# Kernel optimization log

Hardware: AMD Instinct MI355X
Metric: run time of the kernel (lower is better)

Reference implementation:

```python
import jax, jax.numpy as jnp
import numpy as np

B, S, DIM = 2, 1024, 1024
N_EXPERTS, K = 8, 2
VOCAB = 16384
HIDDEN = DIM * 8 // 3          # 2730
UP_OUT = HIDDEN * 2            # 5460 (swiglu doubling)


def setup_inputs() -> dict:
    key = jax.random.key(0)
    ks = jax.random.split(key, 5)
    x = jax.random.normal(ks[0], (B, S, DIM), dtype=jnp.float32)
    w_router = jax.random.normal(ks[1], (N_EXPERTS, DIM), dtype=jnp.float32) * 0.02
    w_up = jax.random.normal(ks[2], (N_EXPERTS, UP_OUT, DIM), dtype=jnp.float32) * 0.02
    w_down = jax.random.normal(ks[3], (N_EXPERTS, DIM, HIDDEN), dtype=jnp.float32) * 0.02
    w_proj = jax.random.normal(ks[4], (N_EXPERTS, VOCAB, DIM), dtype=jnp.float32) * 0.02
    return {"x": x, "w_router": w_router, "w_up": w_up, "w_down": w_down, "w_proj": w_proj}


def _grouped_linear(x_sorted, weight, group_sizes):
    # weight: [n_experts, out, in] (torch Linear layout) -> ragged_dot wants [g, in, out]
    return jax.lax.ragged_dot(x_sorted, jnp.swapaxes(weight, 1, 2), group_sizes)


def reference(x, w_router, w_up, w_down, w_proj):
    b, s, d = x.shape
    # Router (eval path): plain top-k of linear scores
    scores = jnp.einsum("bsd,nd->bsn", x, w_router)
    c, ids = jax.lax.top_k(scores, K)                   # [B,S,K]
    # Dispatch: replicate tokens k times, sort by expert id (stable, matching torch.sort)
    xe = jnp.broadcast_to(x[..., None, :], (b, s, K, d)).reshape(-1, d)   # [T, d]
    ids_flat = ids.reshape(-1)
    order = jnp.argsort(ids_flat)                        # stable sort indices
    x_sorted = xe[order]
    group_sizes = jnp.bincount(ids_flat, length=N_EXPERTS).astype(jnp.int32)
    # Expert swiglu MLP with residual (grouped GEMMs)
    skip = x_sorted
    h = _grouped_linear(x_sorted, w_up, group_sizes)     # [T, 2*HIDDEN]
    h_lin, h_gate = jnp.split(h, 2, axis=-1)
    h = h_lin * jax.nn.silu(h_gate)
    h = _grouped_linear(h, w_down, group_sizes) + skip   # [T, d]
    logits = _grouped_linear(h, w_proj, group_sizes)     # [T, VOCAB]
    # Postprocess: scatter back to original token order
    out = jnp.zeros_like(logits).at[order].set(logits)
    out = out.reshape(b, s, K, VOCAB)
    # Weighted top-k combine
    w = jax.nn.softmax(c, axis=-1)                       # [B,S,K]
    return jnp.sum(out * w[..., None], axis=-2)          # [B,S,VOCAB]
```

## Files before the change

kernel.cpp:

```cpp
#include <hip/hip_runtime.h>
#include <hip/hip_bf16.h>

typedef __bf16 bf16_t;
typedef __bf16 bf16x2 __attribute__((ext_vector_type(2)));
typedef __bf16 bf16x4 __attribute__((ext_vector_type(4)));
typedef __bf16 bf16x8 __attribute__((ext_vector_type(8)));
typedef float f32x4 __attribute__((ext_vector_type(4)));

#define DIM     1024
#define NEXP    8
#define VOCAB   16384
#define HIDDEN  2730
#define UPOUT   5460
#define NTOK    2048
#define NSLOT   4096
#define HRAW_LD 5472
#define H1_LD   2752
#define BM      256
#define MAXTILES 24

#define WS_COUNTS      0
#define WS_NTILES      64
#define WS_TILE_E      128
#define WS_TILE_M0     384
#define WS_TILE_MEND   640
#define WS_SLOT_IDS    1024
#define WS_SLOT_W      17408
#define WS_SLOT_OF_POS 33792
#define WS_POS_OF_SLOT 50176
#define WS_XSORTED     66560
#define WS_H2          8455168
#define WS_H1          16843776
#define WS_HRAW        39388160
#define WS_LOGITS      16843776ull
#define WS_NEED_BIG    (WS_LOGITS + (size_t)NSLOT * VOCAB * 2)

__device__ __forceinline__ void gload_lds16(const void* g, void* l) {
    __builtin_amdgcn_global_load_lds((const __attribute__((address_space(1))) void*)g,
                                     (__attribute__((address_space(3))) void*)l, 16, 0, 0);
}
__device__ __forceinline__ int swz(int r) { return (r ^ (r >> 2)) & 3; }

__global__ __launch_bounds__(256) void router_kernel(const float* __restrict__ x,
        const float* __restrict__ wr, int* __restrict__ slot_ids,
        float* __restrict__ slot_w, int* __restrict__ counts) {
    const int lane = threadIdx.x & 63;
    const int wave = threadIdx.x >> 6;
    const int token = blockIdx.x * 4 + wave;
    const float* xrow = x + (size_t)token * DIM;
    float acc[NEXP];
#pragma unroll
    for (int e = 0; e < NEXP; ++e) acc[e] = 0.f;
#pragma unroll
    for (int i = 0; i < DIM / 64; ++i) {
        const int k = i * 64 + lane;
        const float xv = xrow[k];
#pragma unroll
        for (int e = 0; e < NEXP; ++e) acc[e] += xv * wr[e * DIM + k];
    }
#pragma unroll
    for (int off = 32; off > 0; off >>= 1) {
#pragma unroll
        for (int e = 0; e < NEXP; ++e) acc[e] += __shfl_xor(acc[e], off);
    }
    if (lane == 0) {
        float c0 = -1e30f; int b0 = 0;
#pragma unroll
        for (int e = 0; e < NEXP; ++e) if (acc[e] > c0) { c0 = acc[e]; b0 = e; }
        float c1 = -1e30f; int b1 = 0;
#pragma unroll
        for (int e = 0; e < NEXP; ++e) if (e != b0 && acc[e] > c1) { c1 = acc[e]; b1 = e; }
        slot_ids[token * 2 + 0] = b0;
        slot_ids[token * 2 + 1] = b1;
        const float w0 = 1.f / (1.f + expf(c1 - c0));
        slot_w[token * 2 + 0] = w0;
        slot_w[token * 2 + 1] = 1.f - w0;
        atomicAdd(&counts[b0], 1);
        atomicAdd(&counts[b1], 1);
    }
}

__global__ __launch_bounds__(512) void sched_kernel(const int* __restrict__ counts,
        int* __restrict__ ntiles, int* __restrict__ tile_e, int* __restrict__ tile_m0,
        int* __restrict__ tile_mend, const int* __restrict__ slot_ids,
        int* __restrict__ slot_of_pos, int* __restrict__ pos_of_slot) {
    __shared__ int offs[NEXP];
    if (threadIdx.x == 0) {
        int o = 0, nt = 0;
        for (int e = 0; e < NEXP; ++e) {
            offs[e] = o;
            const int c = counts[e];
            for (int m = 0; m < c; m += BM) {
                tile_e[nt] = e; tile_m0[nt] = o + m; tile_mend[nt] = o + c; ++nt;
            }
            o += c;
        }
        *ntiles = nt;
    }
    __syncthreads();
    const int e = threadIdx.x >> 6;
    const int lane = threadIdx.x & 63;
    int base = offs[e];
    for (int ch = 0; ch < NSLOT / 64; ++ch) {
        const int i = ch * 64 + lane;
        const int id = slot_ids[i];
        const unsigned long long m = __ballot(id == e);
        if (id == e) {
            const int rank = __popcll(m & ((1ull << lane) - 1ull));
            slot_of_pos[base + rank] = i;
            pos_of_slot[i] = base + rank;
        }
        base += __popcll(m);
    }
}

__global__ __launch_bounds__(256) void gather_kernel(const float* __restrict__ x,
        const int* __restrict__ slot_of_pos, bf16_t* __restrict__ xs) {
    const int row = blockIdx.x;
    const int t = threadIdx.x;
    const int tok = slot_of_pos[row] >> 1;
    const float4 v = *(const float4*)(x + (size_t)tok * DIM + t * 4);
    bf16x4 o;
    o.x = (bf16_t)v.x; o.y = (bf16_t)v.y; o.z = (bf16_t)v.z; o.w = (bf16_t)v.w;
    *(bf16x4*)(xs + (size_t)row * DIM + t * 4) = o;
}

__global__ __launch_bounds__(256) void swiglu_kernel(const bf16_t* __restrict__ hraw,
        bf16_t* __restrict__ h1) {
    const int row = blockIdx.x;
    const int col = blockIdx.y * 256 + threadIdx.x;
    if (col >= H1_LD) return;
    float o = 0.f;
    if (col < HIDDEN) {
        const float a = (float)hraw[(size_t)row * HRAW_LD + col];
        const float g = (float)hraw[(size_t)row * HRAW_LD + col + HIDDEN];
        o = a * (g / (1.f + expf(-g)));
    }
    h1[(size_t)row * H1_LD + col] = (bf16_t)o;
}

__global__ __launch_bounds__(256) void combine_kernel(const bf16_t* __restrict__ logits,
        const int* __restrict__ pos_of_slot, const float* __restrict__ slot_w,
        float* __restrict__ out) {
    const int t = blockIdx.x;
    const int v0 = (blockIdx.y * 256 + threadIdx.x) * 8;
    const int p0 = pos_of_slot[2 * t], p1 = pos_of_slot[2 * t + 1];
    const float w0 = slot_w[2 * t], w1 = slot_w[2 * t + 1];
    const bf16x8 a = *(const bf16x8*)(logits + (size_t)p0 * VOCAB + v0);
    const bf16x8 b = *(const bf16x8*)(logits + (size_t)p1 * VOCAB + v0);
    float o[8];
#pragma unroll
    for (int i = 0; i < 8; ++i) o[i] = w0 * (float)a[i] + w1 * (float)b[i];
    *(float4*)(out + (size_t)t * VOCAB + v0)     = make_float4(o[0], o[1], o[2], o[3]);
    *(float4*)(out + (size_t)t * VOCAB + v0 + 4) = make_float4(o[4], o[5], o[6], o[7]);
}

template <int EPI, bool BW16, int BN, bool SWZ>
__global__ __launch_bounds__(1024, 4) void gemm_kernel(
        const bf16_t* __restrict__ A, int lda,
        const float* __restrict__ B, int N, int K, int KT, long bLast,
        bf16_t* __restrict__ C, int ldc,
        const bf16_t* __restrict__ skip,
        const int* __restrict__ slot_of_pos,
        const float* __restrict__ slot_w,
        float* __restrict__ outp,
        const int* __restrict__ tile_e,
        const int* __restrict__ tile_m0,
        const int* __restrict__ tile_mend,
        const int* __restrict__ ntiles) {
    if (blockIdx.y >= (unsigned)*ntiles) return;
    int bx = blockIdx.x;
    if constexpr (SWZ) bx = (bx & 7) * (gridDim.x >> 3) + (bx >> 3);
    const int e = tile_e[blockIdx.y];
    const int m0 = tile_m0[blockIdx.y];
    const int mend = tile_mend[blockIdx.y];
    const int n0 = bx * BN;
    const float* __restrict__ Bexp = B + (size_t)e * N * K;

    constexpr int NI = BN / 64;

    __shared__ bf16_t sA[2][BM][32];
    __shared__ bf16_t sB[2][BN][32];

    const int tid = threadIdx.x;
    const int lane = tid & 63;
    const int wave = tid >> 6;
    const int wr = wave >> 2;
    const int wc = wave & 3;
    const int fr = lane & 15;
    const int fq = lane >> 4;

    f32x4 acc[4][NI] = {};

    auto stageA = [&](int buf, int kt) {
        const int k0 = min(kt, KT - 1) * 32;
        const int rb = wave * 16;
        const int r = rb + (lane >> 2);
        const int gr = min(m0 + r, NSLOT - 1);
        const int c16 = (lane & 3) ^ swz(r);
        gload_lds16(A + (size_t)gr * lda + k0 + c16 * 8, &sA[buf][rb][0]);
    };

    auto loadB = [&](int kt, f32x4& va, float2& vc) {
        const int k0 = min(kt, KT - 1) * 32;
        if constexpr (BW16) {
            const int gr = min(n0 + wave * 8 + (lane >> 3), N - 1);
            va = *(const f32x4*)(Bexp + (size_t)gr * K + k0 + (lane & 7) * 4);
        } else {
            long fl = (long)e * N * K + (long)(n0 + wave * 4 + (lane >> 4)) * K
                      + k0 + (lane & 15) * 2;
            if (fl > bLast) fl = bLast;
            vc = *(const float2*)(B + fl);
        }
    };

    auto writeB = [&](int buf, const f32x4& va, const float2& vc) {
        if constexpr (BW16) {
            const int r = wave * 8 + (lane >> 3);
            bf16x4 t;
            t.x = (bf16_t)va.x; t.y = (bf16_t)va.y;
            t.z = (bf16_t)va.z; t.w = (bf16_t)va.w;
            char* p = (char*)&sB[buf][r][0]
                    + ((((lane & 7) >> 1) ^ swz(r)) * 16) + (lane & 1) * 8;
            *(bf16x4*)p = t;
        } else {
            const int r = wave * 4 + (lane >> 4);
            bf16x2 t; t.x = (bf16_t)vc.x; t.y = (bf16_t)vc.y;
            const int q = lane & 15;
            char* p = (char*)&sB[buf][r][0] + (((q >> 2) ^ swz(r)) * 16) + (q & 3) * 4;
            *(bf16x2*)p = t;
        }
    };

    auto compute = [&](int buf) {
        bf16x8 af[4], bb[NI];
#pragma unroll
        for (int mi = 0; mi < 4; ++mi) {
            const int r = wr * 64 + mi * 16 + fr;
            af[mi] = *(const bf16x8*)&sA[buf][r][(fq ^ swz(r)) * 8];
        }
#pragma unroll
        for (int ni = 0; ni < NI; ++ni) {
            const int r = wc * (BN / 4) + ni * 16 + fr;
            bb[ni] = *(const bf16x8*)&sB[buf][r][(fq ^ swz(r)) * 8];
        }
        __builtin_amdgcn_s_setprio(1);
#pragma unroll
        for (int ni = 0; ni < NI; ++ni)
#pragma unroll
            for (int mi = 0; mi < 4; ++mi)
                acc[mi][ni] = __builtin_amdgcn_mfma_f32_16x16x32_bf16(
                        af[mi], bb[ni], acc[mi][ni], 0, 0, 0);
        __builtin_amdgcn_s_setprio(0);
    };

    f32x4 Pa, Qa; float2 Pc, Qc;
    loadB(0, Pa, Pc);
    stageA(0, 0);
    loadB(1, Qa, Qc);
    asm volatile("s_waitcnt vmcnt(2)" ::: "memory");
    writeB(0, Pa, Pc);
    asm volatile("s_waitcnt lgkmcnt(0)" ::: "memory");
    stageA(1, 1);

    for (int kt = 0; kt < KT; kt += 2) {
        loadB(kt + 2, Pa, Pc);
        asm volatile("s_waitcnt vmcnt(2)" ::: "memory");
        __builtin_amdgcn_s_barrier();
        asm volatile("" ::: "memory");
        writeB(1, Qa, Qc);
        compute(0);
        asm volatile("s_waitcnt lgkmcnt(0)" ::: "memory");
        __builtin_amdgcn_s_barrier();
        asm volatile("" ::: "memory");
        stageA(0, kt + 2);
        loadB(kt + 3, Qa, Qc);
        asm volatile("s_waitcnt vmcnt(2)" ::: "memory");
        __builtin_amdgcn_s_barrier();
        asm volatile("" ::: "memory");
        writeB(0, Pa, Pc);
        compute(1);
        asm volatile("s_waitcnt lgkmcnt(0)" ::: "memory");
        __builtin_amdgcn_s_barrier();
        asm volatile("" ::: "memory");
        stageA(1, kt + 3);
    }

#pragma unroll
    for (int mi = 0; mi < 4; ++mi) {
#pragma unroll
        for (int reg = 0; reg < 4; ++reg) {
            const int r = m0 + wr * 64 + mi * 16 + fq * 4 + reg;
            if (r >= mend) continue;
            int tok = 0; float wgt = 0.f;
            if constexpr (EPI == 2) {
                const int slot = slot_of_pos[r];
                tok = slot >> 1;
                wgt = slot_w[slot];
            }
#pragma unroll
            for (int ni = 0; ni < NI; ++ni) {
                const int c = n0 + wc * (BN / 4) + ni * 16 + fr;
                if (c >= N) continue;
                float v = acc[mi][ni][reg];
                if constexpr (EPI == 0) {
                    C[(size_t)r * ldc + c] = (bf16_t)v;
                } else if constexpr (EPI == 1) {
                    v += (float)skip[(size_t)r * DIM + c];
                    C[(size_t)r * ldc + c] = (bf16_t)v;
                } else if constexpr (EPI == 2) {
                    unsafeAtomicAdd(&outp[(size_t)tok * VOCAB + c], v * wgt);
                } else {
                    C[(size_t)r * VOCAB + c] = (bf16_t)v;
                }
            }
        }
    }
}

extern "C" void kernel_launch(void* const* d_in, const int* in_sizes, int n_in,
                              void* d_out, int out_size, void* d_ws, size_t ws_size,
                              hipStream_t stream) {
    const float* x        = (const float*)d_in[0];
    const float* w_router = (const float*)d_in[1];
    const float* w_up     = (const float*)d_in[2];
    const float* w_down   = (const float*)d_in[3];
    const float* w_proj   = (const float*)d_in[4];
    float* out = (float*)d_out;
    char* ws = (char*)d_ws;

    int*    counts      = (int*)(ws + WS_COUNTS);
    int*    ntiles      = (int*)(ws + WS_NTILES);
    int*    tile_e      = (int*)(ws + WS_TILE_E);
    int*    tile_m0     = (int*)(ws + WS_TILE_M0);
    int*    tile_mend   = (int*)(ws + WS_TILE_MEND);
    int*    slot_ids    = (int*)(ws + WS_SLOT_IDS);
    float*  slot_w      = (float*)(ws + WS_SLOT_W);
    int*    slot_of_pos = (int*)(ws + WS_SLOT_OF_POS);
    int*    pos_of_slot = (int*)(ws + WS_POS_OF_SLOT);
    bf16_t* x_sorted    = (bf16_t*)(ws + WS_XSORTED);
    bf16_t* h2          = (bf16_t*)(ws + WS_H2);
    bf16_t* h1          = (bf16_t*)(ws + WS_H1);
    bf16_t* h_raw       = (bf16_t*)(ws + WS_HRAW);
    bf16_t* logits      = (bf16_t*)(ws + WS_LOGITS);

    const bool bigws = ws_size >= WS_NEED_BIG;

    hipMemsetAsync(d_ws, 0, 1024, stream);

    router_kernel<<<NTOK / 4, 256, 0, stream>>>(x, w_router, slot_ids, slot_w, counts);
    sched_kernel<<<1, 512, 0, stream>>>(counts, ntiles, tile_e, tile_m0, tile_mend,
                                        slot_ids, slot_of_pos, pos_of_slot);
    gather_kernel<<<NSLOT, 256, 0, stream>>>(x, slot_of_pos, x_sorted);

    gemm_kernel<0, true, 128, false><<<dim3((UPOUT + 127) / 128, MAXTILES), 1024, 0, stream>>>(
        x_sorted, DIM, w_up, UPOUT, DIM, 32, 0,
        h_raw, HRAW_LD,
        nullptr, nullptr, nullptr, nullptr, tile_e, tile_m0, tile_mend, ntiles);

    swiglu_kernel<<<dim3(NSLOT, (H1_LD + 255) / 256), 256, 0, stream>>>(h_raw, h1);

    gemm_kernel<1, false, 64, true><<<dim3(DIM / 64, MAXTILES), 1024, 0, stream>>>(
        h1, H1_LD, w_down, DIM, HIDDEN, (HIDDEN + 31) / 32,
        (long)NEXP * DIM * HIDDEN - 2,
        h2, DIM,
        x_sorted, nullptr, nullptr, nullptr, tile_e, tile_m0, tile_mend, ntiles);

    if (bigws) {
        gemm_kernel<3, true, 128, true><<<dim3(VOCAB / 128, MAXTILES), 1024, 0, stream>>>(
            h2, DIM, w_proj, VOCAB, DIM, 32, 0,
            logits, VOCAB,
            nullptr, nullptr, nullptr, nullptr, tile_e, tile_m0, tile_mend, ntiles);
        combine_kernel<<<dim3(NTOK, VOCAB / (256 * 8)), 256, 0, stream>>>(
            logits, pos_of_slot, slot_w, out);
    } else {
        hipMemsetAsync(d_out, 0, (size_t)out_size * sizeof(float), stream);
        gemm_kernel<2, true, 128, true><<<dim3(VOCAB / 128, MAXTILES), 1024, 0, stream>>>(
            h2, DIM, w_proj, VOCAB, DIM, 32, 0,
            nullptr, 0,
            nullptr, slot_of_pos, slot_w, out, tile_e, tile_m0, tile_mend, ntiles);
    }
}
```

Baseline: 747.2 us.

## Add 256x256 K-64 pipelined GEMM for up and vocab projections

Adds a new grouped GEMM kernel, gemm_big, with 512 threads, 256x256 output tiles and 64-wide K steps. Its main loop is split into four MFMA quadrants, with B global loads, A direct-to-LDS DMA and the B fp32-to-bf16 LDS writes interleaved between them and fenced by explicit barriers and sched_barriers. It is used for the up projection and the vocab projection, where K is 1024; the down projection keeps the old kernel, renamed gemm_mid. The aim is more operand reuse per tile and less fp32 weight reload traffic. The cost is higher register and LDS use (128 KB of LDS per block) and many more barriers per K step.

```diff
diff --git a/kernel.cpp b/kernel.cpp
--- a/kernel.cpp
+++ b/kernel.cpp
@@ -39,7 +39,7 @@
     __builtin_amdgcn_global_load_lds((const __attribute__((address_space(1))) void*)g,
                                      (__attribute__((address_space(3))) void*)l, 16, 0, 0);
 }
-__device__ __forceinline__ int swz(int r) { return (r ^ (r >> 2)) & 3; }
+__device__ __forceinline__ int swzm(int r) { return (r ^ (r >> 2)) & 3; }
 
 __global__ __launch_bounds__(256) void router_kernel(const float* __restrict__ x,
         const float* __restrict__ wr, int* __restrict__ slot_ids,
@@ -155,8 +155,186 @@
     *(float4*)(out + (size_t)t * VOCAB + v0 + 4) = make_float4(o[4], o[5], o[6], o[7]);
 }
 
+template <int EPI>
+__global__ __launch_bounds__(512, 2) void gemm_big(
+        const bf16_t* __restrict__ A,
+        const float* __restrict__ B, int N,
+        bf16_t* __restrict__ C, int ldc,
+        const int* __restrict__ slot_of_pos,
+        const float* __restrict__ slot_w,
+        float* __restrict__ outp,
+        const int* __restrict__ tile_e,
+        const int* __restrict__ tile_m0,
+        const int* __restrict__ tile_mend,
+        const int* __restrict__ ntiles) {
+    if (blockIdx.y >= (unsigned)*ntiles) return;
+    constexpr int K = 1024, KT = 16;
+    const int e = tile_e[blockIdx.y];
+    const int m0 = tile_m0[blockIdx.y];
+    const int mend = tile_mend[blockIdx.y];
+    const int n0 = blockIdx.x * 256;
+
+    __shared__ bf16_t sA[2][256][64];
+    __shared__ bf16_t sB[2][256][64];
+
+    const int tid = threadIdx.x;
+    const int lane = tid & 63;
+    const int wave = tid >> 6;
+    const int wr = wave >> 2;
+    const int wc = wave & 3;
+    const int fr = lane & 15;
+    const int fq = lane >> 4;
+
+    const int brow = tid >> 1;
+    const int bhalf = tid & 1;
+    const int bswz = brow & 7;
+    const float* bsrc = B + (size_t)e * N * K + (size_t)min(n0 + brow, N - 1) * K
+                          + bhalf * 32;
+
+    f32x4 acc[8][4] = {};
+    bf16x8 af[4][2], bb[4][2];
+    f32x4 l[8];
+
+    auto dmaA = [&](int buf, int t, int j) {
+        const int k0 = min(t, KT - 1) * 64;
+        const int rb = j * 64 + wave * 8;
+        const int r  = rb + (lane >> 3);
+        const int gr = min(m0 + r, NSLOT - 1);
+        const int su = (lane & 7) ^ (r & 7);
+        gload_lds16(A + (size_t)gr * K + k0 + su * 8, &sA[buf][rb][0]);
+    };
+    auto loadB4 = [&](int t, int base) {
+        const int k0 = min(t, KT - 1) * 64;
+#pragma unroll
+        for (int j = 0; j < 4; ++j)
+            l[base + j] = *(const f32x4*)(bsrc + k0 + (base + j) * 4);
+    };
+    auto writeB = [&](int buf, int w) {
+        bf16x8 t;
+        t[0] = (bf16_t)l[2*w][0]; t[1] = (bf16_t)l[2*w][1];
+        t[2] = (bf16_t)l[2*w][2]; t[3] = (bf16_t)l[2*w][3];
+        t[4] = (bf16_t)l[2*w+1][0]; t[5] = (bf16_t)l[2*w+1][1];
+        t[6] = (bf16_t)l[2*w+1][2]; t[7] = (bf16_t)l[2*w+1][3];
+        const int us = (bhalf * 4 + w) ^ bswz;
+        *(bf16x8*)&sB[buf][brow][us * 8] = t;
+    };
+    auto readA = [&](int buf, int mh) {
+#pragma unroll
+        for (int kk = 0; kk < 2; ++kk)
+#pragma unroll
+            for (int mi = 0; mi < 4; ++mi) {
+                const int r = wr * 128 + mh * 64 + mi * 16 + fr;
+                af[mi][kk] = *(const bf16x8*)&sA[buf][r][((kk * 4 + fq) ^ (r & 7)) * 8];
+            }
+    };
+    auto readB = [&](int buf, int nh) {
+#pragma unroll
+        for (int kk = 0; kk < 2; ++kk)
+#pragma unroll
+            for (int ni = 0; ni < 2; ++ni) {
+                const int r = wc * 64 + nh * 32 + ni * 16 + fr;
+                bb[nh * 2 + ni][kk] =
+                    *(const bf16x8*)&sB[buf][r][((kk * 4 + fq) ^ (r & 7)) * 8];
+            }
+    };
+    auto quad = [&](int mh, int nh) {
+        __builtin_amdgcn_s_setprio(1);
+#pragma unroll
+        for (int kk = 0; kk < 2; ++kk)
+#pragma unroll
+            for (int ni = 0; ni < 2; ++ni)
+#pragma unroll
+                for (int mi = 0; mi < 4; ++mi)
+                    acc[mh * 4 + mi][nh * 2 + ni] =
+                        __builtin_amdgcn_mfma_f32_16x16x32_bf16(
+                            af[mi][kk], bb[nh * 2 + ni][kk],
+                            acc[mh * 4 + mi][nh * 2 + ni], 0, 0, 0);
+        __builtin_amdgcn_s_setprio(0);
+    };
+
+    loadB4(0, 0); loadB4(0, 4);
+#pragma unroll
+    for (int j = 0; j < 4; ++j) dmaA(0, 0, j);
+    writeB(0, 0); writeB(0, 1); writeB(0, 2); writeB(0, 3);
+    asm volatile("s_waitcnt vmcnt(0)" ::: "memory");
+    asm volatile("s_waitcnt lgkmcnt(0)" ::: "memory");
+    __builtin_amdgcn_s_barrier();
+    asm volatile("" ::: "memory");
+
+    for (int t = 0; t < KT; ++t) {
+        const int cur = t & 1;
+        readA(cur, 0); readB(cur, 0);
+        loadB4(t + 1, 0);
+#pragma unroll
+        for (int j = 0; j < 4; ++j) dmaA(cur ^ 1, t + 1, j);
+        asm volatile("" ::: "memory");
+        __builtin_amdgcn_s_barrier();
+        asm volatile("s_waitcnt lgkmcnt(0)" ::: "memory");
+        __builtin_amdgcn_sched_barrier(0);
+        quad(0, 0);
+        asm volatile("" ::: "memory");
+        __builtin_amdgcn_s_barrier();
+        readB(cur, 1);
+        loadB4(t + 1, 4);
+        asm volatile("" ::: "memory");
+        __builtin_amdgcn_s_barrier();
+        asm volatile("s_waitcnt lgkmcnt(0)" ::: "memory");
+        __builtin_amdgcn_sched_barrier(0);
+        quad(0, 1);
+        asm volatile("" ::: "memory");
+        __builtin_amdgcn_s_barrier();
+        asm volatile("s_waitcnt vmcnt(8)" ::: "memory");
+        writeB(cur ^ 1, 0); writeB(cur ^ 1, 1);
+        readA(cur, 1);
+        asm volatile("" ::: "memory");
+        __builtin_amdgcn_s_barrier();
+        asm volatile("s_waitcnt lgkmcnt(0)" ::: "memory");
+        __builtin_amdgcn_sched_barrier(0);
+        quad(1, 0);
+        asm volatile("" ::: "memory");
+        __builtin_amdgcn_s_barrier();
+        asm volatile("s_waitcnt vmcnt(0)" ::: "memory");
+        writeB(cur ^ 1, 2); writeB(cur ^ 1, 3);
+        asm volatile("" ::: "memory");
+        __builtin_amdgcn_s_barrier();
+        asm volatile("s_waitcnt lgkmcnt(0)" ::: "memory");
+        __builtin_amdgcn_sched_barrier(0);
+        quad(1, 1);
+        asm volatile("" ::: "memory");
+        __builtin_amdgcn_s_barrier();
+    }
+
+#pragma unroll
+    for (int a = 0; a < 8; ++a) {
+#pragma unroll
+        for (int reg = 0; reg < 4; ++reg) {
+            const int r = m0 + wr * 128 + (a >> 2) * 64 + (a & 3) * 16 + fq * 4 + reg;
+            if (r >= mend) continue;
+            int tok = 0; float wgt = 0.f;
+            if constexpr (EPI == 2) {
+                const int slot = slot_of_pos[r];
+                tok = slot >> 1;
+                wgt = slot_w[slot];
+            }
+#pragma unroll
+            for (int b = 0; b < 4; ++b) {
+                const int c = n0 + wc * 64 + (b >> 1) * 32 + (b & 1) * 16 + fr;
+                if (c >= N) continue;
+                float v = acc[a][b][reg];
+                if constexpr (EPI == 0) {
+                    C[(size_t)r * ldc + c] = (bf16_t)v;
+                } else if constexpr (EPI == 2) {
+                    unsafeAtomicAdd(&outp[(size_t)tok * VOCAB + c], v * wgt);
+                } else {
+                    C[(size_t)r * VOCAB + c] = (bf16_t)v;
+                }
+            }
+        }
+    }
+}
+
 template <int EPI, bool BW16, int BN, bool SWZ>
-__global__ __launch_bounds__(1024, 4) void gemm_kernel(
+__global__ __launch_bounds__(1024, 4) void gemm_mid(
         const bf16_t* __restrict__ A, int lda,
         const float* __restrict__ B, int N, int K, int KT, long bLast,
         bf16_t* __restrict__ C, int ldc,
@@ -175,7 +353,6 @@
     const int m0 = tile_m0[blockIdx.y];
     const int mend = tile_mend[blockIdx.y];
     const int n0 = bx * BN;
-    const float* __restrict__ Bexp = B + (size_t)e * N * K;
 
     constexpr int NI = BN / 64;
 
@@ -197,15 +374,14 @@
         const int rb = wave * 16;
         const int r = rb + (lane >> 2);
         const int gr = min(m0 + r, NSLOT - 1);
-        const int c16 = (lane & 3) ^ swz(r);
+        const int c16 = (lane & 3) ^ swzm(r);
         gload_lds16(A + (size_t)gr * lda + k0 + c16 * 8, &sA[buf][rb][0]);
     };
-
     auto loadB = [&](int kt, f32x4& va, float2& vc) {
         const int k0 = min(kt, KT - 1) * 32;
         if constexpr (BW16) {
-            const int gr = min(n0 + wave * 8 + (lane >> 3), N - 1);
-            va = *(const f32x4*)(Bexp + (size_t)gr * K + k0 + (lane & 7) * 4);
+            va = *(const f32x4*)(B + (size_t)e * N * K
+                 + (size_t)min(n0 + wave * 8 + (lane >> 3), N - 1) * K + k0 + (lane & 7) * 4);
         } else {
             long fl = (long)e * N * K + (long)(n0 + wave * 4 + (lane >> 4)) * K
                       + k0 + (lane & 15) * 2;
@@ -213,7 +389,6 @@
             vc = *(const float2*)(B + fl);
         }
     };
-
     auto writeB = [&](int buf, const f32x4& va, const float2& vc) {
         if constexpr (BW16) {
             const int r = wave * 8 + (lane >> 3);
@@ -221,28 +396,27 @@
             t.x = (bf16_t)va.x; t.y = (bf16_t)va.y;
             t.z = (bf16_t)va.z; t.w = (bf16_t)va.w;
             char* p = (char*)&sB[buf][r][0]
-                    + ((((lane & 7) >> 1) ^ swz(r)) * 16) + (lane & 1) * 8;
+                    + ((((lane & 7) >> 1) ^ swzm(r)) * 16) + (lane & 1) * 8;
             *(bf16x4*)p = t;
         } else {
             const int r = wave * 4 + (lane >> 4);
             bf16x2 t; t.x = (bf16_t)vc.x; t.y = (bf16_t)vc.y;
             const int q = lane & 15;
-            char* p = (char*)&sB[buf][r][0] + (((q >> 2) ^ swz(r)) * 16) + (q & 3) * 4;
+            char* p = (char*)&sB[buf][r][0] + (((q >> 2) ^ swzm(r)) * 16) + (q & 3) * 4;
             *(bf16x2*)p = t;
         }
     };
-
     auto compute = [&](int buf) {
         bf16x8 af[4], bb[NI];
 #pragma unroll
         for (int mi = 0; mi < 4; ++mi) {
             const int r = wr * 64 + mi * 16 + fr;
-            af[mi] = *(const bf16x8*)&sA[buf][r][(fq ^ swz(r)) * 8];
+            af[mi] = *(const bf16x8*)&sA[buf][r][(fq ^ swzm(r)) * 8];
         }
 #pragma unroll
         for (int ni = 0; ni < NI; ++ni) {
             const int r = wc * (BN / 4) + ni * 16 + fr;
-            bb[ni] = *(const bf16x8*)&sB[buf][r][(fq ^ swz(r)) * 8];
+            bb[ni] = *(const bf16x8*)&sB[buf][r][(fq ^ swzm(r)) * 8];
         }
         __builtin_amdgcn_s_setprio(1);
 #pragma unroll
@@ -292,26 +466,16 @@
         for (int reg = 0; reg < 4; ++reg) {
             const int r = m0 + wr * 64 + mi * 16 + fq * 4 + reg;
             if (r >= mend) continue;
-            int tok = 0; float wgt = 0.f;
-            if constexpr (EPI == 2) {
-                const int slot = slot_of_pos[r];
-                tok = slot >> 1;
-                wgt = slot_w[slot];
-            }
 #pragma unroll
             for (int ni = 0; ni < NI; ++ni) {
                 const int c = n0 + wc * (BN / 4) + ni * 16 + fr;
                 if (c >= N) continue;
                 float v = acc[mi][ni][reg];
-                if constexpr (EPI == 0) {
-                    C[(size_t)r * ldc + c] = (bf16_t)v;
-                } else if constexpr (EPI == 1) {
+                if constexpr (EPI == 1) {
                     v += (float)skip[(size_t)r * DIM + c];
                     C[(size_t)r * ldc + c] = (bf16_t)v;
-                } else if constexpr (EPI == 2) {
-                    unsafeAtomicAdd(&outp[(size_t)tok * VOCAB + c], v * wgt);
                 } else {
-                    C[(size_t)r * VOCAB + c] = (bf16_t)v;
+                    C[(size_t)r * ldc + c] = (bf16_t)v;
                 }
             }
         }
@@ -353,31 +517,28 @@
                                         slot_ids, slot_of_pos, pos_of_slot);
     gather_kernel<<<NSLOT, 256, 0, stream>>>(x, slot_of_pos, x_sorted);
 
-    gemm_kernel<0, true, 128, false><<<dim3((UPOUT + 127) / 128, MAXTILES), 1024, 0, stream>>>(
-        x_sorted, DIM, w_up, UPOUT, DIM, 32, 0,
-        h_raw, HRAW_LD,
-        nullptr, nullptr, nullptr, nullptr, tile_e, tile_m0, tile_mend, ntiles);
+    gemm_big<0><<<dim3((UPOUT + 255) / 256, MAXTILES), 512, 0, stream>>>(
+        x_sorted, w_up, UPOUT, h_raw, HRAW_LD,
+        nullptr, nullptr, nullptr, tile_e, tile_m0, tile_mend, ntiles);
 
     swiglu_kernel<<<dim3(NSLOT, (H1_LD + 255) / 256), 256, 0, stream>>>(h_raw, h1);
 
-    gemm_kernel<1, false, 64, true><<<dim3(DIM / 64, MAXTILES), 1024, 0, stream>>>(
+    gemm_mid<1, false, 64, true><<<dim3(DIM / 64, MAXTILES), 1024, 0, stream>>>(
         h1, H1_LD, w_down, DIM, HIDDEN, (HIDDEN + 31) / 32,
         (long)NEXP * DIM * HIDDEN - 2,
         h2, DIM,
         x_sorted, nullptr, nullptr, nullptr, tile_e, tile_m0, tile_mend, ntiles);
 
     if (bigws) {
-        gemm_kernel<3, true, 128, true><<<dim3(VOCAB / 128, MAXTILES), 1024, 0, stream>>>(
-            h2, DIM, w_proj, VOCAB, DIM, 32, 0,
-            logits, VOCAB,
-            nullptr, nullptr, nullptr, nullptr, tile_e, tile_m0, tile_mend, ntiles);
+        gemm_big<3><<<dim3(VOCAB / 256, MAXTILES), 512, 0, stream>>>(
+            h2, w_proj, VOCAB, logits, VOCAB,
+            nullptr, nullptr, nullptr, tile_e, tile_m0, tile_mend, ntiles);
         combine_kernel<<<dim3(NTOK, VOCAB / (256 * 8)), 256, 0, stream>>>(
             logits, pos_of_slot, slot_w, out);
     } else {
         hipMemsetAsync(d_out, 0, (size_t)out_size * sizeof(float), stream);
-        gemm_kernel<2, true, 128, true><<<dim3(VOCAB / 128, MAXTILES), 1024, 0, stream>>>(
-            h2, DIM, w_proj, VOCAB, DIM, 32, 0,
-            nullptr, 0,
-            nullptr, slot_of_pos, slot_w, out, tile_e, tile_m0, tile_mend, ntiles);
-    }
-}
+        gemm_big<2><<<dim3(VOCAB / 256, MAXTILES), 512, 0, stream>>>(
+            h2, w_proj, VOCAB, nullptr, 0,
+            slot_of_pos, slot_w, out, tile_e, tile_m0, tile_mend, ntiles);
+    }
+}
```

Result: slower. 785.3 us (+5.1%).
